# Optimization experiments

Hardware: AMD Instinct MI355X
Metric: run time of the kernel (lower is better)

The kernel has to match this reference:

```python
import jax, jax.numpy as jnp
from jax import lax
import numpy as np

B, L, C_IN, HID, RANK, NC = 256, 1024, 16, 512, 128, 10
PAD, K = 4, 7  # each conv block: L -> L + 2*PAD - K + 1 = L + 2


def _block(x, dwk, dwb, pwk, pwb, g, b):
    # x: (B, C, L); depthwise conv (groups=C) -> pointwise 1x1 -> batchnorm (batch stats) -> relu
    cin = dwk.shape[0]
    dn = ('NCH', 'OIH', 'NCH')
    y = lax.conv_general_dilated(x, dwk, (1,), [(PAD, PAD)], dimension_numbers=dn,
                                 feature_group_count=cin) + dwb[None, :, None]
    y = lax.conv_general_dilated(y, pwk, (1,), [(0, 0)], dimension_numbers=dn) + pwb[None, :, None]
    m = y.mean(axis=(0, 2), keepdims=True)
    v = y.var(axis=(0, 2), keepdims=True)
    y = (y - m) * lax.rsqrt(v + 1e-5) * g[None, :, None] + b[None, :, None]
    return jax.nn.relu(y)


def _cell(xp, h, c, Ui, Vi, Uh, Vh, bi, bh):
    # low-rank LSTM cell: W = U @ V kept factored for efficiency (same math)
    gates = (xp @ Ui) @ Vi + bi + (h @ Uh) @ Vh + bh  # (B, 4H)
    i, f, g, o = jnp.split(gates, 4, axis=1)
    c = jax.nn.sigmoid(f) * c + jax.nn.sigmoid(i) * jnp.tanh(g)
    h = jax.nn.sigmoid(o) * jnp.tanh(c)
    return h, c


def _forward(x, dw_k1, dw_b1, pw_k1, pw_b1, bn_g1, bn_b1,
             dw_k2, dw_b2, pw_k2, pw_b2, bn_g2, bn_b2,
             dw_k3, dw_b3, pw_k3, pw_b3, bn_g3, bn_b3,
             dw_k4, dw_b4, pw_k4, pw_b4, bn_g4, bn_b4,
             Ui1, Vi1, Uh1, Vh1, bi1, bh1,
             Ui2, Vi2, Uh2, Vh2, bi2, bh2,
             fc_w, fc_b):
    y = x[:, 0].transpose(0, 2, 1)  # (B, C_IN, L)
    y = _block(y, dw_k1, dw_b1, pw_k1, pw_b1, bn_g1, bn_b1)
    y = _block(y, dw_k2, dw_b2, pw_k2, pw_b2, bn_g2, bn_b2)
    y = _block(y, dw_k3, dw_b3, pw_k3, pw_b3, bn_g3, bn_b3)
    y = _block(y, dw_k4, dw_b4, pw_k4, pw_b4, bn_g4, bn_b4)
    # dropout = identity (eval)
    xs = y.transpose(2, 0, 1)  # (T, B, 32), T = L + 8
    bsz = xs.shape[1]
    z = jnp.zeros((bsz, HID), xs.dtype)

    def step(carry, xt):
        h1, c1, h2, c2 = carry
        h1, c1 = _cell(xt, h1, c1, Ui1, Vi1, Uh1, Vh1, bi1, bh1)
        h2, c2 = _cell(h1, h2, c2, Ui2, Vi2, Uh2, Vh2, bi2, bh2)
        return (h1, c1, h2, c2), None

    (h1, c1, h2, c2), _ = lax.scan(step, (z, z, z, z), xs)
    # original stacks all h2 then takes [:, -1, :] -> final h2; dropout = identity
    return h2 @ fc_w.T + fc_b  # (B, NC)


def setup_inputs() -> dict:
    key = jax.random.key(0)
    ks = iter(jax.random.split(key, 64))

    def n(shape, scale=0.05):
        return jax.random.normal(next(ks), shape, jnp.float32) * scale

    inp = {'x': jax.random.normal(next(ks), (B, 1, L, C_IN), jnp.float32)}
    chans = [C_IN, 32, 32, 32]
    for i, cin in enumerate(chans, start=1):
        inp[f'dw_k{i}'] = n((cin, 1, K))
        inp[f'dw_b{i}'] = jnp.zeros((cin,), jnp.float32)
        inp[f'pw_k{i}'] = n((32, cin, 1))
        inp[f'pw_b{i}'] = jnp.zeros((32,), jnp.float32)
        inp[f'bn_g{i}'] = jnp.ones((32,), jnp.float32)
        inp[f'bn_b{i}'] = jnp.zeros((32,), jnp.float32)
    inp['Ui1'] = n((32, RANK)); inp['Vi1'] = n((RANK, 4 * HID))
    inp['Uh1'] = n((HID, RANK)); inp['Vh1'] = n((RANK, 4 * HID))
    inp['bi1'] = jnp.zeros((4 * HID,), jnp.float32); inp['bh1'] = jnp.zeros((4 * HID,), jnp.float32)
    inp['Ui2'] = n((HID, RANK)); inp['Vi2'] = n((RANK, 4 * HID))
    inp['Uh2'] = n((HID, RANK)); inp['Vh2'] = n((RANK, 4 * HID))
    inp['bi2'] = jnp.zeros((4 * HID,), jnp.float32); inp['bh2'] = jnp.zeros((4 * HID,), jnp.float32)
    inp['fc_w'] = n((NC, HID)); inp['fc_b'] = jnp.zeros((NC,), jnp.float32)
    return inp


def reference(x, dw_k1, dw_b1, pw_k1, pw_b1, bn_g1, bn_b1,
              dw_k2, dw_b2, pw_k2, pw_b2, bn_g2, bn_b2,
              dw_k3, dw_b3, pw_k3, pw_b3, bn_g3, bn_b3,
              dw_k4, dw_b4, pw_k4, pw_b4, bn_g4, bn_b4,
              Ui1, Vi1, Uh1, Vh1, bi1, bh1,
              Ui2, Vi2, Uh2, Vh2, bi2, bh2,
              fc_w, fc_b):
    return _forward(x, dw_k1, dw_b1, pw_k1, pw_b1, bn_g1, bn_b1,
                    dw_k2, dw_b2, pw_k2, pw_b2, bn_g2, bn_b2,
                    dw_k3, dw_b3, pw_k3, pw_b3, bn_g3, bn_b3,
                    dw_k4, dw_b4, pw_k4, pw_b4, bn_g4, bn_b4,
                    Ui1, Vi1, Uh1, Vh1, bi1, bh1,
                    Ui2, Vi2, Uh2, Vh2, bi2, bh2,
                    fc_w, fc_b)
```

## Files before the change

### kernel.cpp

```cpp
#include <hip/hip_runtime.h>
#include <stdint.h>
#include <stddef.h>
#include <limits.h>

typedef _Float16 f16;
typedef _Float16 half8 __attribute__((ext_vector_type(8)));
typedef float floatx4 __attribute__((ext_vector_type(4)));
typedef unsigned long long u64;

#define MFMA(a,b,c) __builtin_amdgcn_mfma_f32_16x16x32_f16((a),(b),(c),0,0,0)

static constexpr int LMAX   = 1032;
static constexpr int TSTEPS = 1032;

static constexpr size_t ZBYTES   = (size_t)256*32*LMAX*2;
static constexpr size_t OFF_ZA   = 0;
static constexpr size_t OFF_ZB   = OFF_ZA + ZBYTES;
static constexpr size_t OFF_Y4   = OFF_ZA;
static constexpr size_t OFF_WH1F = OFF_ZB + ZBYTES;
static constexpr size_t OFF_WI2F = OFF_WH1F + (size_t)128*16*64*8*2;
static constexpr size_t OFF_WH2F = OFF_WI2F + (size_t)128*16*64*8*2;
static constexpr size_t OFF_WX1F = OFF_WH2F + (size_t)128*16*64*8*2;
static constexpr size_t OFF_B1   = OFF_WX1F + (size_t)128*64*8*2;
static constexpr size_t OFF_B2   = OFF_B1 + (size_t)2048*4;
static constexpr size_t OFF_STATS= OFF_B2 + (size_t)2048*4;
static constexpr size_t OFF_AB   = OFF_STATS + (size_t)4*64*4;
static constexpr size_t OFF_H1X  = OFF_AB + (size_t)4*64*4;
static constexpr size_t OFF_H2X  = OFF_H1X + (size_t)8*8*32*512*2;
static constexpr size_t OFF_FLAGS= OFF_H2X + (size_t)8*4*32*512*2;

__device__ __forceinline__ float sigm(float x){ return 1.f/(1.f+__expf(-x)); }
__device__ __forceinline__ float tanh_f(float x){ float e=__expf(2.f*x); return (e-1.f)/(e+1.f); }

__device__ __forceinline__ void sta64(void* p, u64 v){
  __hip_atomic_store((u64*)p, v, __ATOMIC_RELAXED, __HIP_MEMORY_SCOPE_AGENT);
}
__device__ __forceinline__ u64 lda64(const void* p){
  return __hip_atomic_load((const u64*)p, __ATOMIC_RELAXED, __HIP_MEMORY_SCOPE_AGENT);
}
__device__ __forceinline__ uint32_t ldf(const uint32_t* p){
  return __hip_atomic_load(p, __ATOMIC_RELAXED, __HIP_MEMORY_SCOPE_AGENT);
}
__device__ __forceinline__ void stf(uint32_t* p, uint32_t v){
  __hip_atomic_store(p, v, __ATOMIC_RELAXED, __HIP_MEMORY_SCOPE_AGENT);
}
__device__ __forceinline__ float4 ldg16(const void* p){
  float4 r;
  asm volatile("global_load_dwordx4 %0, %1, off sc0 sc1" : "=v"(r) : "v"(p) : "memory");
  return r;
}
__device__ __forceinline__ void vmcnt0(){
  asm volatile("s_waitcnt vmcnt(0)" ::: "memory");
}

__device__ __forceinline__ void pollWave(const uint32_t* fl, int t1, int t2){
  const int lane = threadIdx.x & 63;
  int tgt = (lane < 16) ? t1 : ((lane < 32) ? t2 : INT_MIN);
  if (tgt <= 0) tgt = INT_MIN;
  while (true){
    uint32_t v = ldf(&fl[lane & 31]);
    if (__all((int)v >= tgt)) break;
    __builtin_amdgcn_s_sleep(1);
  }
}

__device__ __forceinline__ void stageIssue(float4* r, const f16* src, int tid){
  #pragma unroll
  for (int i=0;i<8;++i){
    int qq = tid + 256*i;
    r[i] = ldg16(src + (size_t)qq*8);
  }
}
__device__ __forceinline__ void stageWrite(uint8_t* base, const float4* r, int tid){
  #pragma unroll
  for (int i=0;i<8;++i){
    int qq = tid + 256*i;
    int row = qq >> 6, ck = qq & 63;
    int cs = ck ^ (row & 15);
    *(float4*)(base + ((row<<6) + cs)*16) = r[i];
  }
}
__device__ __forceinline__ half8 fragLDS(const uint8_t* base, int row, int q, int lq){
  return *(const half8*)(base + (((row<<6)) + (((q<<2)+lq) ^ (row & 15)))*16);
}

__global__ void k_zero(float* stats, uint32_t* flags){
  int bx = blockIdx.x, tid = threadIdx.x;
  if (bx == 4){ if (tid < 256) stats[tid] = 0.f; }
  else flags[bx*256 + tid] = 0u;
}

__global__ __launch_bounds__(256) void k_prep_W(f16* __restrict__ dst, const float* __restrict__ U, const float* __restrict__ V){
  __shared__ float sU[64][65];
  __shared__ float sV[64][68];
  const int tid = threadIdx.x;
  const int n0 = blockIdx.x*64, k0 = blockIdx.y*64;
  const int tx = tid & 15, ty = tid >> 4;
  float acc[4][4];
  #pragma unroll
  for (int a=0;a<4;++a){ acc[a][0]=0.f; acc[a][1]=0.f; acc[a][2]=0.f; acc[a][3]=0.f; }
  for (int rc=0; rc<2; ++rc){
    __syncthreads();
    #pragma unroll
    for (int i=0;i<16;++i){
      int f = tid + 256*i;
      int row = f>>6, col = f&63;
      sU[row][col] = U[(size_t)(k0+row)*128 + rc*64 + col];
      sV[row][col] = V[(size_t)(rc*64+row)*2048 + n0 + col];
    }
    __syncthreads();
    for (int rr=0; rr<64; ++rr){
      float4 bv = *(const float4*)&sV[rr][tx*4];
      #pragma unroll
      for (int a=0;a<4;++a){
        float av = sU[ty*4+a][rr];
        acc[a][0] += av*bv.x; acc[a][1] += av*bv.y; acc[a][2] += av*bv.z; acc[a][3] += av*bv.w;
      }
    }
  }
  #pragma unroll
  for (int a=0;a<4;++a){
    int k = k0 + ty*4 + a;
    int q = k>>5, lq2 = (k>>3)&3, j = k&7;
    #pragma unroll
    for (int c=0;c<4;++c){
      int n = n0 + tx*4 + c;
      int nt = n>>4, lmn = n&15;
      dst[(((size_t)nt*16 + q)*64 + (lq2*16+lmn))*8 + j] = (f16)acc[a][c];
    }
  }
}

__global__ __launch_bounds__(256) void k_prep_Wx(f16* __restrict__ dst, const float* __restrict__ U, const float* __restrict__ V){
  __shared__ float sU[32][129];
  __shared__ float sV[128][68];
  const int tid = threadIdx.x, n0 = blockIdx.x*64;
  for (int f=tid; f<32*128; f+=256) sU[f>>7][f&127] = U[f];
  for (int f=tid; f<128*64; f+=256) sV[f>>6][f&63] = V[(size_t)(f>>6)*2048 + n0 + (f&63)];
  __syncthreads();
  int nn = tid & 63, kb = (tid>>6)*8;
  int n = n0 + nn;
  float acc[8];
  #pragma unroll
  for (int i=0;i<8;++i) acc[i]=0.f;
  for (int r=0;r<128;++r){
    float v = sV[r][nn];
    #pragma unroll
    for (int i=0;i<8;++i) acc[i] += sU[kb+i][r]*v;
  }
  int nt = n>>4, lmn = n&15;
  #pragma unroll
  for (int i=0;i<8;++i){
    int k = kb+i;
    dst[((size_t)nt*64 + (((k>>3)&3)*16 + lmn))*8 + (k&7)] = (f16)acc[i];
  }
}

__global__ void k_prep_bias(float* dst, const float* a, const float* b){
  int idx = blockIdx.x*256 + threadIdx.x;
  if (idx < 2048) dst[idx] = a[idx] + b[idx];
}

__global__ __launch_bounds__(256) void k_conv(
    const float* __restrict__ x0, const f16* __restrict__ zin,
    const float* __restrict__ abp,
    const float* __restrict__ dwk, const float* __restrict__ dwb,
    const float* __restrict__ pwk, const float* __restrict__ pwb,
    f16* __restrict__ zout, float* __restrict__ stats,
    int Lin, int Cin)
{
  const int tid = threadIdx.x;
  const int b = blockIdx.y;
  const int l = blockIdx.x*256 + tid;
  const int Lout = Lin + 2;
  __shared__ float sPw[32*32], sDw[32*7], sDb[32], sPb[32], sAb[64];
  __shared__ float sRed[2][4][32];
  for (int i=tid; i<Cin*32; i+=256) sPw[i] = pwk[i];
  for (int i=tid; i<Cin*7;  i+=256) sDw[i] = dwk[i];
  if (tid < Cin) sDb[tid] = dwb[tid];
  if (tid >= 64 && tid < 96) sPb[tid-64] = pwb[tid-64];
  if (abp != nullptr && tid >= 128 && tid < 192) sAb[tid-128] = abp[tid-128];
  __syncthreads();

  float acc[32];
  #pragma unroll
  for (int o=0;o<32;++o) acc[o] = sPb[o];
  const bool act = (l < Lout);
  if (act){
    for (int c=0;c<Cin;++c){
      float s = sDb[c];
      #pragma unroll
      for (int k=0;k<7;++k){
        int li = l + k - 4;
        float v = 0.f;
        if (li >= 0 && li < Lin){
          if (x0) v = x0[((size_t)b*1024 + li)*16 + c];
          else {
            float z = (float)zin[((size_t)b*32 + c)*LMAX + li];
            v = fmaxf(sAb[c]*z + sAb[32+c], 0.f);
          }
        }
        s += sDw[c*7+k]*v;
      }
      #pragma unroll
      for (int o=0;o<32;++o) acc[o] += sPw[o*Cin + c]*s;
    }
    #pragma unroll
    for (int o=0;o<32;++o) zout[((size_t)b*32 + o)*LMAX + l] = (f16)acc[o];
  }
  const int lane = tid & 63, wv = tid >> 6;
  for (int o=0;o<32;++o){
    float v = act ? acc[o] : 0.f;
    float q = v*v;
    #pragma unroll
    for (int m=1;m<64;m<<=1){ v += __shfl_xor(v,m); q += __shfl_xor(q,m); }
    if (lane == 0){ sRed[0][wv][o] = v; sRed[1][wv][o] = q; }
  }
  __syncthreads();
  if (tid < 32){
    float v = sRed[0][0][tid]+sRed[0][1][tid]+sRed[0][2][tid]+sRed[0][3][tid];
    float q = sRed[1][0][tid]+sRed[1][1][tid]+sRed[1][2][tid]+sRed[1][3][tid];
    atomicAdd(&stats[tid], v);
    atomicAdd(&stats[32+tid], q);
  }
}

__global__ void k_bnfin(const float* __restrict__ stats, const float* __restrict__ g,
                        const float* __restrict__ beta, float* __restrict__ ab, float inv_n)
{
  int o = threadIdx.x;
  if (o < 32){
    float m = stats[o]*inv_n;
    float var = stats[32+o]*inv_n - m*m;
    float a = g[o]*rsqrtf(var + 1e-5f);
    ab[o] = a; ab[32+o] = beta[o] - m*a;
  }
}

__global__ __launch_bounds__(256) void k_y4(const f16* __restrict__ z, const float* __restrict__ ab, f16* __restrict__ y){
  __shared__ f16 sT[32][264];
  __shared__ float sA[64];
  const int b = blockIdx.x, t0 = blockIdx.y*256, tid = threadIdx.x;
  if (tid < 64) sA[tid] = ab[tid];
  __syncthreads();
  #pragma unroll
  for (int i=0;i<8;++i){
    int f = tid + 256*i;
    int ch = f >> 6, tq = f & 63;
    int t = t0 + tq*4;
    if (t < 1032){
      u64 v = *(const u64*)(z + ((size_t)(b*32+ch)*1032 + t));
      union { u64 u; f16 h[4]; } cv; cv.u = v;
      float a = sA[ch], bb = sA[32+ch];
      #pragma unroll
      for (int j=0;j<4;++j) cv.h[j] = (f16)fmaxf(a*(float)cv.h[j] + bb, 0.f);
      *(u64*)&sT[ch][tq*4] = cv.u;
    }
  }
  __syncthreads();
  int t = t0 + tid;
  if (t < 1032){
    union { uint4 v; f16 h[8]; } o[4];
    #pragma unroll
    for (int k=0;k<4;++k)
      #pragma unroll
      for (int j=0;j<8;++j) o[k].h[j] = sT[k*8+j][t - t0];
    uint4* dst = (uint4*)(y + ((size_t)b*1032 + t)*32);
    #pragma unroll
    for (int k=0;k<4;++k) dst[k] = o[k].v;
  }
}

__global__ __launch_bounds__(256,1) void k_lstm(
  const f16* __restrict__ y4x,
  const f16* __restrict__ Wx1F, const f16* __restrict__ Wh1F,
  const f16* __restrict__ Wi2F, const f16* __restrict__ Wh2F,
  const float* __restrict__ bias1, const float* __restrict__ bias2,
  f16* __restrict__ h1x, f16* __restrict__ h2x,
  uint32_t* __restrict__ flags,
  const float* __restrict__ fcw, const float* __restrict__ fcb,
  float* __restrict__ outp)
{
  const int tid  = threadIdx.x;
  const int lane = tid & 63;
  const int w    = tid >> 6;
  const int lm   = lane & 15;
  const int lq   = lane >> 4;
  const int lq8  = lq*8;
  const int g    = blockIdx.x & 7;
  const int idx  = blockIdx.x >> 3;
  const int role = idx >> 4;
  const int b    = idx & 15;

  __shared__ __align__(16) uint8_t bufA[32768];
  __shared__ __align__(16) uint8_t bufB[32768];
  __shared__ float sGate[4*32*33];

  uint32_t* fl = flags + (size_t)g*32;

  const float* biasL = role ? bias2 : bias1;
  float bs[2];
  #pragma unroll
  for (int ct=0; ct<2; ++ct) bs[ct] = biasL[w*512 + b*32 + ct*16 + lm];

  const int nt0 = w*32 + b*2;
  f16* hdst_base = role ? h2x + (size_t)g*4*32*512 : h1x + (size_t)g*8*32*512;

  float creg[4] = {0.f,0.f,0.f,0.f};
  const int cr_row = tid >> 3, cr_u0 = (tid & 7)*4;

  if (role == 0){
    half8 wx[2];
    half8 wB[2][16];
    #pragma unroll
    for (int ct=0; ct<2; ++ct){
      wx[ct] = *(const half8*)&Wx1F[((size_t)(nt0+ct)*64 + lane)*8];
      #pragma unroll
      for (int q=0;q<16;++q)
        wB[ct][q] = *(const half8*)&Wh1F[(((size_t)(nt0+ct)*16 + q)*64 + lane)*8];
    }
    #pragma unroll 1
    for (int t=0; t<TSTEPS; ++t){
      half8 ya0 = *(const half8*)(y4x + ((size_t)(g*32 + lm)*1032 + t)*32 + lq8);
      half8 ya1 = *(const half8*)(y4x + ((size_t)(g*32 + 16 + lm)*1032 + t)*32 + lq8);
      if (w == 0) pollWave(fl, t, t-7);
      __syncthreads();
      float4 st[8];
      if (t >= 1) stageIssue(st, h1x + ((size_t)(g*8 + ((t-1)&7))*32*512), tid);
      floatx4 acc[2][2];
      #pragma unroll
      for (int ct=0; ct<2; ++ct){
        acc[ct][0] = (floatx4){bs[ct],bs[ct],bs[ct],bs[ct]};
        acc[ct][1] = acc[ct][0];
      }
      acc[0][0] = MFMA(ya0, wx[0], acc[0][0]);
      acc[0][1] = MFMA(ya1, wx[0], acc[0][1]);
      acc[1][0] = MFMA(ya0, wx[1], acc[1][0]);
      acc[1][1] = MFMA(ya1, wx[1], acc[1][1]);
      if (t >= 1){
        vmcnt0();
        stageWrite(bufA, st, tid);
      }
      __syncthreads();
      if (t >= 1){
        #pragma unroll
        for (int q=0;q<16;++q){
          half8 a0 = fragLDS(bufA, lm,    q, lq);
          half8 a1 = fragLDS(bufA, 16+lm, q, lq);
          acc[0][0] = MFMA(a0, wB[0][q], acc[0][0]);
          acc[0][1] = MFMA(a1, wB[0][q], acc[0][1]);
          acc[1][0] = MFMA(a0, wB[1][q], acc[1][0]);
          acc[1][1] = MFMA(a1, wB[1][q], acc[1][1]);
        }
      }
      __syncthreads();
      #pragma unroll
      for (int ct=0; ct<2; ++ct)
        #pragma unroll
        for (int rt=0; rt<2; ++rt)
          #pragma unroll
          for (int r=0;r<4;++r)
            sGate[w*1056 + (rt*16 + lq*4 + r)*33 + ct*16 + lm] = acc[ct][rt][r];
      __syncthreads();
      {
        union { u64 uu; f16 h[4]; } hv;
        #pragma unroll
        for (int j=0;j<4;++j){
          int u = cr_u0 + j;
          float iv = sGate[0*1056 + cr_row*33 + u];
          float fv = sGate[1*1056 + cr_row*33 + u];
          float gv = sGate[2*1056 + cr_row*33 + u];
          float ov = sGate[3*1056 + cr_row*33 + u];
          float c = sigm(fv)*creg[j] + sigm(iv)*tanh_f(gv);
          creg[j] = c;
          hv.h[j] = (f16)(sigm(ov)*tanh_f(c));
        }
        f16* dst = hdst_base + (size_t)(t&7)*32*512 + cr_row*512 + b*32 + cr_u0;
        sta64(dst, hv.uu);
      }
      vmcnt0();
      __syncthreads();
      if (tid == 0) stf(&fl[b], (uint32_t)(t+1));
    }
  } else {
    half8 wA[2][16];
    half8 wB[2][16];
    #pragma unroll
    for (int ct=0; ct<2; ++ct)
      #pragma unroll
      for (int q=0;q<16;++q){
        wA[ct][q] = *(const half8*)&Wi2F[(((size_t)(nt0+ct)*16 + q)*64 + lane)*8];
        wB[ct][q] = *(const half8*)&Wh2F[(((size_t)(nt0+ct)*16 + q)*64 + lane)*8];
      }
    #pragma unroll 1
    for (int t=0; t<TSTEPS; ++t){
      if (w == 0) pollWave(fl, t+1, t);
      __syncthreads();
      float4 s0[8], s1[8];
      stageIssue(s0, h1x + ((size_t)(g*8 + (t&7))*32*512), tid);
      if (t >= 1) stageIssue(s1, h2x + ((size_t)(g*4 + ((t-1)&3))*32*512), tid);
      vmcnt0();
      stageWrite(bufA, s0, tid);
      if (t >= 1) stageWrite(bufB, s1, tid);
      __syncthreads();
      floatx4 acc[2][2];
      #pragma unroll
      for (int ct=0; ct<2; ++ct){
        acc[ct][0] = (floatx4){bs[ct],bs[ct],bs[ct],bs[ct]};
        acc[ct][1] = acc[ct][0];
      }
      #pragma unroll
      for (int q=0;q<16;++q){
        half8 a0 = fragLDS(bufA, lm,    q, lq);
        half8 a1 = fragLDS(bufA, 16+lm, q, lq);
        acc[0][0] = MFMA(a0, wA[0][q], acc[0][0]);
        acc[0][1] = MFMA(a1, wA[0][q], acc[0][1]);
        acc[1][0] = MFMA(a0, wA[1][q], acc[1][0]);
        acc[1][1] = MFMA(a1, wA[1][q], acc[1][1]);
      }
      if (t >= 1){
        #pragma unroll
        for (int q=0;q<16;++q){
          half8 a0 = fragLDS(bufB, lm,    q, lq);
          half8 a1 = fragLDS(bufB, 16+lm, q, lq);
          acc[0][0] = MFMA(a0, wB[0][q], acc[0][0]);
          acc[0][1] = MFMA(a1, wB[0][q], acc[0][1]);
          acc[1][0] = MFMA(a0, wB[1][q], acc[1][0]);
          acc[1][1] = MFMA(a1, wB[1][q], acc[1][1]);
        }
      }
      __syncthreads();
      #pragma unroll
      for (int ct=0; ct<2; ++ct)
        #pragma unroll
        for (int rt=0; rt<2; ++rt)
          #pragma unroll
          for (int r=0;r<4;++r)
            sGate[w*1056 + (rt*16 + lq*4 + r)*33 + ct*16 + lm] = acc[ct][rt][r];
      __syncthreads();
      {
        union { u64 uu; f16 h[4]; } hv;
        #pragma unroll
        for (int j=0;j<4;++j){
          int u = cr_u0 + j;
          float iv = sGate[0*1056 + cr_row*33 + u];
          float fv = sGate[1*1056 + cr_row*33 + u];
          float gv = sGate[2*1056 + cr_row*33 + u];
          float ov = sGate[3*1056 + cr_row*33 + u];
          float c = sigm(fv)*creg[j] + sigm(iv)*tanh_f(gv);
          creg[j] = c;
          hv.h[j] = (f16)(sigm(ov)*tanh_f(c));
        }
        f16* dst = hdst_base + (size_t)(t&3)*32*512 + cr_row*512 + b*32 + cr_u0;
        sta64(dst, hv.uu);
      }
      vmcnt0();
      __syncthreads();
      if (tid == 0) stf(&fl[16 + b], (uint32_t)(t+1));
    }
    if (b == 0){
      if (w == 0) pollWave(fl, 0, TSTEPS);
      __syncthreads();
      const f16* hbase = h2x + ((size_t)(g*4 + ((TSTEPS-1)&3))*32*512);
      for (int e = tid; e < 320; e += 256){
        int row = e/10, nc = e%10;
        float s = fcb[nc];
        const float* wv = fcw + (size_t)nc*512;
        const u64* hp = (const u64*)(hbase + row*512);
        for (int k4=0;k4<128;++k4){
          union { u64 uu; f16 h[4]; } cv; cv.uu = lda64(hp + k4);
          #pragma unroll
          for (int i2=0;i2<4;++i2) s += (float)cv.h[i2]*wv[k4*4+i2];
        }
        outp[(size_t)(g*32+row)*10 + nc] = s;
      }
    }
  }
}

extern "C" void kernel_launch(void* const* d_in, const int* in_sizes, int n_in,
                              void* d_out, int out_size, void* d_ws, size_t ws_size,
                              hipStream_t stream)
{
  (void)in_sizes; (void)n_in; (void)out_size; (void)ws_size;
  const float* x = (const float*)d_in[0];
  auto F = [&](int i){ return (const float*)d_in[i]; };
  const float *Ui1=F(25), *Vi1=F(26), *Uh1=F(27), *Vh1=F(28), *bi1=F(29), *bh1=F(30);
  const float *Ui2=F(31), *Vi2=F(32), *Uh2=F(33), *Vh2=F(34), *bi2=F(35), *bh2=F(36);
  const float *fcw=F(37), *fcb=F(38);

  uint8_t* ws = (uint8_t*)d_ws;
  f16* zA   = (f16*)(ws + OFF_ZA);
  f16* zB   = (f16*)(ws + OFF_ZB);
  f16* y4x  = (f16*)(ws + OFF_Y4);
  f16* Wh1F = (f16*)(ws + OFF_WH1F);
  f16* Wi2F = (f16*)(ws + OFF_WI2F);
  f16* Wh2F = (f16*)(ws + OFF_WH2F);
  f16* Wx1F = (f16*)(ws + OFF_WX1F);
  float* bias1 = (float*)(ws + OFF_B1);
  float* bias2 = (float*)(ws + OFF_B2);
  float* stats = (float*)(ws + OFF_STATS);
  float* ab    = (float*)(ws + OFF_AB);
  f16* h1x  = (f16*)(ws + OFF_H1X);
  f16* h2x  = (f16*)(ws + OFF_H2X);
  uint32_t* flags = (uint32_t*)(ws + OFF_FLAGS);
  float* outp = (float*)d_out;

  k_zero<<<5, 256, 0, stream>>>(stats, flags);

  k_prep_W<<<dim3(32,8), 256, 0, stream>>>(Wh1F, Uh1, Vh1);
  k_prep_W<<<dim3(32,8), 256, 0, stream>>>(Wi2F, Ui2, Vi2);
  k_prep_W<<<dim3(32,8), 256, 0, stream>>>(Wh2F, Uh2, Vh2);
  k_prep_Wx<<<32, 256, 0, stream>>>(Wx1F, Ui1, Vi1);
  k_prep_bias<<<8, 256, 0, stream>>>(bias1, bi1, bh1);
  k_prep_bias<<<8, 256, 0, stream>>>(bias2, bi2, bh2);

  dim3 cgrid(5, 256);
  k_conv<<<cgrid, 256, 0, stream>>>(x, nullptr, nullptr, F(1), F(2), F(3), F(4),
                                    zA, stats + 0*64, 1024, 16);
  k_bnfin<<<1, 64, 0, stream>>>(stats + 0*64, F(5), F(6), ab + 0*64, 1.f/(256.f*1026.f));
  k_conv<<<cgrid, 256, 0, stream>>>(nullptr, zA, ab + 0*64, F(7), F(8), F(9), F(10),
                                    zB, stats + 1*64, 1026, 32);
  k_bnfin<<<1, 64, 0, stream>>>(stats + 1*64, F(11), F(12), ab + 1*64, 1.f/(256.f*1028.f));
  k_conv<<<cgrid, 256, 0, stream>>>(nullptr, zB, ab + 1*64, F(13), F(14), F(15), F(16),
                                    zA, stats + 2*64, 1028, 32);
  k_bnfin<<<1, 64, 0, stream>>>(stats + 2*64, F(17), F(18), ab + 2*64, 1.f/(256.f*1030.f));
  k_conv<<<cgrid, 256, 0, stream>>>(nullptr, zA, ab + 2*64, F(19), F(20), F(21), F(22),
                                    zB, stats + 3*64, 1030, 32);
  k_bnfin<<<1, 64, 0, stream>>>(stats + 3*64, F(23), F(24), ab + 3*64, 1.f/(256.f*1032.f));

  k_y4<<<dim3(256,5), 256, 0, stream>>>(zB, ab + 3*64, y4x);

  k_lstm<<<256, 256, 0, stream>>>(y4x,
                                  Wx1F, Wh1F, Wi2F, Wh2F,
                                  bias1, bias2,
                                  h1x, h2x, flags,
                                  fcw, fcb, outp);
}
```

Measured before the change: 6.149 ms.

## Replace flag-based handoff with sequence-tagged ring entries in LSTM pipeline

Each hidden-state word written to the global ring buffers now carries the timestep in its upper 32 bits, so consumers poll the data itself rather than waiting for a per-block flag. This removes the producer-side vmcnt wait, barrier and flag store in layer 1, and the consumer-side flag poll before staging. Layer 2 also prefetches the h1 ring while doing its h2 MFMAs. The cost is doubled ring traffic (each 4-byte payload sits in an 8-byte word), a larger zero-init kernel for the rings, and retry loops whenever tags are stale.

```diff
diff --git a/kernel.cpp b/kernel.cpp
--- a/kernel.cpp
+++ b/kernel.cpp
@@ -26,8 +26,8 @@
 static constexpr size_t OFF_STATS= OFF_B2 + (size_t)2048*4;
 static constexpr size_t OFF_AB   = OFF_STATS + (size_t)4*64*4;
 static constexpr size_t OFF_H1X  = OFF_AB + (size_t)4*64*4;
-static constexpr size_t OFF_H2X  = OFF_H1X + (size_t)8*8*32*512*2;
-static constexpr size_t OFF_FLAGS= OFF_H2X + (size_t)8*4*32*512*2;
+static constexpr size_t OFF_H2X  = OFF_H1X + (size_t)8*8*8192*8;
+static constexpr size_t OFF_FLAGS= OFF_H2X + (size_t)8*4*8192*8;
 
 __device__ __forceinline__ float sigm(float x){ return 1.f/(1.f+__expf(-x)); }
 __device__ __forceinline__ float tanh_f(float x){ float e=__expf(2.f*x); return (e-1.f)/(e+1.f); }
@@ -44,50 +44,54 @@
 __device__ __forceinline__ void stf(uint32_t* p, uint32_t v){
   __hip_atomic_store(p, v, __ATOMIC_RELAXED, __HIP_MEMORY_SCOPE_AGENT);
 }
-__device__ __forceinline__ float4 ldg16(const void* p){
-  float4 r;
-  asm volatile("global_load_dwordx4 %0, %1, off sc0 sc1" : "=v"(r) : "v"(p) : "memory");
-  return r;
-}
-__device__ __forceinline__ void vmcnt0(){
-  asm volatile("s_waitcnt vmcnt(0)" ::: "memory");
-}
-
-__device__ __forceinline__ void pollWave(const uint32_t* fl, int t1, int t2){
+
+__device__ __forceinline__ void pollCons(const uint32_t* fl, int tgt){
   const int lane = threadIdx.x & 63;
-  int tgt = (lane < 16) ? t1 : ((lane < 32) ? t2 : INT_MIN);
-  if (tgt <= 0) tgt = INT_MIN;
+  int t2 = (lane < 16) ? tgt : INT_MIN;
   while (true){
-    uint32_t v = ldf(&fl[lane & 31]);
-    if (__all((int)v >= tgt)) break;
-    __builtin_amdgcn_s_sleep(1);
-  }
-}
-
-__device__ __forceinline__ void stageIssue(float4* r, const f16* src, int tid){
-  #pragma unroll
-  for (int i=0;i<8;++i){
-    int qq = tid + 256*i;
-    r[i] = ldg16(src + (size_t)qq*8);
-  }
-}
-__device__ __forceinline__ void stageWrite(uint8_t* base, const float4* r, int tid){
-  #pragma unroll
-  for (int i=0;i<8;++i){
-    int qq = tid + 256*i;
-    int row = qq >> 6, ck = qq & 63;
-    int cs = ck ^ (row & 15);
-    *(float4*)(base + ((row<<6) + cs)*16) = r[i];
-  }
-}
-__device__ __forceinline__ half8 fragLDS(const uint8_t* base, int row, int q, int lq){
-  return *(const half8*)(base + (((row<<6)) + (((q<<2)+lq) ^ (row & 15)))*16);
-}
-
-__global__ void k_zero(float* stats, uint32_t* flags){
+    uint32_t v = ldf(&fl[16 + (lane & 15)]);
+    if (__all((int)v >= t2)) break;
+    __builtin_amdgcn_s_sleep(2);
+  }
+}
+
+__device__ __forceinline__ void issueChunks(u64* v, const u64* slot, int tid){
+  const int base = (tid>>3)*256 + (tid&7)*2;
+  #pragma unroll
+  for (int i=0;i<16;++i){
+    v[2*i]   = lda64(slot + base + 16*i);
+    v[2*i+1] = lda64(slot + base + 16*i + 1);
+  }
+}
+__device__ __forceinline__ bool finishChunks(uint8_t* lds, const u64* v, int tid, uint32_t expect){
+  const int r = tid>>3, c0 = (tid&7)*2;
+  bool ok = true;
+  #pragma unroll
+  for (int i=0;i<16;++i){
+    u64 a = v[2*i], b = v[2*i+1];
+    ok &= ((uint32_t)(a>>32) == expect);
+    ok &= ((uint32_t)(b>>32) == expect);
+    *(uint2*)(lds + r*1040 + (c0 + 16*i)*4) = make_uint2((uint32_t)a, (uint32_t)b);
+  }
+  return ok;
+}
+__device__ __forceinline__ void stageLoop(uint8_t* lds, const u64* slot, int tid, uint32_t expect){
+  while (true){
+    u64 v[32];
+    issueChunks(v, slot, tid);
+    bool ok = finishChunks(lds, v, tid, expect);
+    if (__syncthreads_and(ok)) break;
+    __builtin_amdgcn_s_sleep(4);
+  }
+}
+__device__ __forceinline__ half8 fragP(const uint8_t* base, int row, int q, int lq){
+  return *(const half8*)(base + row*1040 + (((q<<2)+lq)<<4));
+}
+
+__global__ void k_zero(float* stats, uint32_t* flags, uint4* rings){
   int bx = blockIdx.x, tid = threadIdx.x;
-  if (bx == 4){ if (tid < 256) stats[tid] = 0.f; }
-  else flags[bx*256 + tid] = 0u;
+  if (bx < 1536) rings[(size_t)bx*256 + tid] = (uint4){0u,0u,0u,0u};
+  else { stats[tid] = 0.f; flags[tid] = 0u; }
 }
 
 __global__ __launch_bounds__(256) void k_prep_W(f16* __restrict__ dst, const float* __restrict__ U, const float* __restrict__ V){
@@ -276,7 +280,7 @@
   const f16* __restrict__ Wx1F, const f16* __restrict__ Wh1F,
   const f16* __restrict__ Wi2F, const f16* __restrict__ Wh2F,
   const float* __restrict__ bias1, const float* __restrict__ bias2,
-  f16* __restrict__ h1x, f16* __restrict__ h2x,
+  u64* __restrict__ h1x, u64* __restrict__ h2x,
   uint32_t* __restrict__ flags,
   const float* __restrict__ fcw, const float* __restrict__ fcb,
   float* __restrict__ outp)
@@ -292,10 +296,12 @@
   const int role = idx >> 4;
   const int b    = idx & 15;
 
-  __shared__ __align__(16) uint8_t bufA[32768];
-  __shared__ __align__(16) uint8_t bufB[32768];
+  __shared__ __align__(16) uint8_t bufA[33280];
+  __shared__ __align__(16) uint8_t bufB[33280];
   __shared__ float sGate[4*32*33];
 
+  u64* ring1 = h1x + (size_t)g*8*8192;
+  u64* ring2 = h2x + (size_t)g*4*8192;
   uint32_t* fl = flags + (size_t)g*32;
 
   const float* biasL = role ? bias2 : bias1;
@@ -304,10 +310,10 @@
   for (int ct=0; ct<2; ++ct) bs[ct] = biasL[w*512 + b*32 + ct*16 + lm];
 
   const int nt0 = w*32 + b*2;
-  f16* hdst_base = role ? h2x + (size_t)g*4*32*512 : h1x + (size_t)g*8*32*512;
 
   float creg[4] = {0.f,0.f,0.f,0.f};
   const int cr_row = tid >> 3, cr_u0 = (tid & 7)*4;
+  const int chunkBase = cr_row*256 + b*16 + (tid & 7)*2;
 
   if (role == 0){
     half8 wx[2];
@@ -323,10 +329,8 @@
     for (int t=0; t<TSTEPS; ++t){
       half8 ya0 = *(const half8*)(y4x + ((size_t)(g*32 + lm)*1032 + t)*32 + lq8);
       half8 ya1 = *(const half8*)(y4x + ((size_t)(g*32 + 16 + lm)*1032 + t)*32 + lq8);
-      if (w == 0) pollWave(fl, t, t-7);
+      if (w == 0 && t >= 8) pollCons(fl, t-7);
       __syncthreads();
-      float4 st[8];
-      if (t >= 1) stageIssue(st, h1x + ((size_t)(g*8 + ((t-1)&7))*32*512), tid);
       floatx4 acc[2][2];
       #pragma unroll
       for (int ct=0; ct<2; ++ct){
@@ -338,22 +342,17 @@
       acc[1][0] = MFMA(ya0, wx[1], acc[1][0]);
       acc[1][1] = MFMA(ya1, wx[1], acc[1][1]);
       if (t >= 1){
-        vmcnt0();
-        stageWrite(bufA, st, tid);
-      }
-      __syncthreads();
-      if (t >= 1){
+        stageLoop(bufA, ring1 + (size_t)((t-1)&7)*8192, tid, (uint32_t)t);
         #pragma unroll
         for (int q=0;q<16;++q){
-          half8 a0 = fragLDS(bufA, lm,    q, lq);
-          half8 a1 = fragLDS(bufA, 16+lm, q, lq);
+          half8 a0 = fragP(bufA, lm,    q, lq);
+          half8 a1 = fragP(bufA, 16+lm, q, lq);
           acc[0][0] = MFMA(a0, wB[0][q], acc[0][0]);
           acc[0][1] = MFMA(a1, wB[0][q], acc[0][1]);
           acc[1][0] = MFMA(a0, wB[1][q], acc[1][0]);
           acc[1][1] = MFMA(a1, wB[1][q], acc[1][1]);
         }
       }
-      __syncthreads();
       #pragma unroll
       for (int ct=0; ct<2; ++ct)
         #pragma unroll
@@ -363,7 +362,7 @@
             sGate[w*1056 + (rt*16 + lq*4 + r)*33 + ct*16 + lm] = acc[ct][rt][r];
       __syncthreads();
       {
-        union { u64 uu; f16 h[4]; } hv;
+        union { u64 uu; f16 h[4]; uint32_t u32v[2]; } hv;
         #pragma unroll
         for (int j=0;j<4;++j){
           int u = cr_u0 + j;
@@ -375,12 +374,11 @@
           creg[j] = c;
           hv.h[j] = (f16)(sigm(ov)*tanh_f(c));
         }
-        f16* dst = hdst_base + (size_t)(t&7)*32*512 + cr_row*512 + b*32 + cr_u0;
-        sta64(dst, hv.uu);
-      }
-      vmcnt0();
-      __syncthreads();
-      if (tid == 0) stf(&fl[b], (uint32_t)(t+1));
+        u64 seqw = ((u64)(uint32_t)(t+1)) << 32;
+        u64* dst = ring1 + (size_t)(t&7)*8192 + chunkBase;
+        sta64(dst,     (u64)hv.u32v[0] | seqw);
+        sta64(dst + 1, (u64)hv.u32v[1] | seqw);
+      }
     }
   } else {
     half8 wA[2][16];
@@ -394,42 +392,40 @@
       }
     #pragma unroll 1
     for (int t=0; t<TSTEPS; ++t){
-      if (w == 0) pollWave(fl, t+1, t);
-      __syncthreads();
-      float4 s0[8], s1[8];
-      stageIssue(s0, h1x + ((size_t)(g*8 + (t&7))*32*512), tid);
-      if (t >= 1) stageIssue(s1, h2x + ((size_t)(g*4 + ((t-1)&3))*32*512), tid);
-      vmcnt0();
-      stageWrite(bufA, s0, tid);
-      if (t >= 1) stageWrite(bufB, s1, tid);
-      __syncthreads();
       floatx4 acc[2][2];
       #pragma unroll
       for (int ct=0; ct<2; ++ct){
         acc[ct][0] = (floatx4){bs[ct],bs[ct],bs[ct],bs[ct]};
         acc[ct][1] = acc[ct][0];
       }
-      #pragma unroll
-      for (int q=0;q<16;++q){
-        half8 a0 = fragLDS(bufA, lm,    q, lq);
-        half8 a1 = fragLDS(bufA, 16+lm, q, lq);
-        acc[0][0] = MFMA(a0, wA[0][q], acc[0][0]);
-        acc[0][1] = MFMA(a1, wA[0][q], acc[0][1]);
-        acc[1][0] = MFMA(a0, wA[1][q], acc[1][0]);
-        acc[1][1] = MFMA(a1, wA[1][q], acc[1][1]);
-      }
       if (t >= 1){
+        stageLoop(bufB, ring2 + (size_t)((t-1)&3)*8192, tid, (uint32_t)t);
+        u64 vh[32];
+        issueChunks(vh, ring1 + (size_t)(t&7)*8192, tid);
         #pragma unroll
         for (int q=0;q<16;++q){
-          half8 a0 = fragLDS(bufB, lm,    q, lq);
-          half8 a1 = fragLDS(bufB, 16+lm, q, lq);
+          half8 a0 = fragP(bufB, lm,    q, lq);
+          half8 a1 = fragP(bufB, 16+lm, q, lq);
           acc[0][0] = MFMA(a0, wB[0][q], acc[0][0]);
           acc[0][1] = MFMA(a1, wB[0][q], acc[0][1]);
           acc[1][0] = MFMA(a0, wB[1][q], acc[1][0]);
           acc[1][1] = MFMA(a1, wB[1][q], acc[1][1]);
         }
-      }
-      __syncthreads();
+        bool ok = finishChunks(bufA, vh, tid, (uint32_t)(t+1));
+        if (!__syncthreads_and(ok))
+          stageLoop(bufA, ring1 + (size_t)(t&7)*8192, tid, (uint32_t)(t+1));
+      } else {
+        stageLoop(bufA, ring1 + 0, tid, 1u);
+      }
+      #pragma unroll
+      for (int q=0;q<16;++q){
+        half8 a0 = fragP(bufA, lm,    q, lq);
+        half8 a1 = fragP(bufA, 16+lm, q, lq);
+        acc[0][0] = MFMA(a0, wA[0][q], acc[0][0]);
+        acc[0][1] = MFMA(a1, wA[0][q], acc[0][1]);
+        acc[1][0] = MFMA(a0, wA[1][q], acc[1][0]);
+        acc[1][1] = MFMA(a1, wA[1][q], acc[1][1]);
+      }
       #pragma unroll
       for (int ct=0; ct<2; ++ct)
         #pragma unroll
@@ -439,7 +435,7 @@
             sGate[w*1056 + (rt*16 + lq*4 + r)*33 + ct*16 + lm] = acc[ct][rt][r];
       __syncthreads();
       {
-        union { u64 uu; f16 h[4]; } hv;
+        union { u64 uu; f16 h[4]; uint32_t u32v[2]; } hv;
         #pragma unroll
         for (int j=0;j<4;++j){
           int u = cr_u0 + j;
@@ -451,27 +447,21 @@
           creg[j] = c;
           hv.h[j] = (f16)(sigm(ov)*tanh_f(c));
         }
-        f16* dst = hdst_base + (size_t)(t&3)*32*512 + cr_row*512 + b*32 + cr_u0;
-        sta64(dst, hv.uu);
-      }
-      vmcnt0();
-      __syncthreads();
+        u64 seqw = ((u64)(uint32_t)(t+1)) << 32;
+        u64* dst = ring2 + (size_t)(t&3)*8192 + chunkBase;
+        sta64(dst,     (u64)hv.u32v[0] | seqw);
+        sta64(dst + 1, (u64)hv.u32v[1] | seqw);
+      }
       if (tid == 0) stf(&fl[16 + b], (uint32_t)(t+1));
     }
     if (b == 0){
-      if (w == 0) pollWave(fl, 0, TSTEPS);
-      __syncthreads();
-      const f16* hbase = h2x + ((size_t)(g*4 + ((TSTEPS-1)&3))*32*512);
+      stageLoop(bufA, ring2 + (size_t)((TSTEPS-1)&3)*8192, tid, (uint32_t)TSTEPS);
       for (int e = tid; e < 320; e += 256){
         int row = e/10, nc = e%10;
         float s = fcb[nc];
         const float* wv = fcw + (size_t)nc*512;
-        const u64* hp = (const u64*)(hbase + row*512);
-        for (int k4=0;k4<128;++k4){
-          union { u64 uu; f16 h[4]; } cv; cv.uu = lda64(hp + k4);
-          #pragma unroll
-          for (int i2=0;i2<4;++i2) s += (float)cv.h[i2]*wv[k4*4+i2];
-        }
+        const f16* hp = (const f16*)(bufA + row*1040);
+        for (int u=0;u<512;++u) s += (float)hp[u]*wv[u];
         outp[(size_t)(g*32+row)*10 + nc] = s;
       }
     }
@@ -501,12 +491,12 @@
   float* bias2 = (float*)(ws + OFF_B2);
   float* stats = (float*)(ws + OFF_STATS);
   float* ab    = (float*)(ws + OFF_AB);
-  f16* h1x  = (f16*)(ws + OFF_H1X);
-  f16* h2x  = (f16*)(ws + OFF_H2X);
+  u64* h1x  = (u64*)(ws + OFF_H1X);
+  u64* h2x  = (u64*)(ws + OFF_H2X);
   uint32_t* flags = (uint32_t*)(ws + OFF_FLAGS);
   float* outp = (float*)d_out;
 
-  k_zero<<<5, 256, 0, stream>>>(stats, flags);
+  k_zero<<<1537, 256, 0, stream>>>(stats, flags, (uint4*)h1x);
 
   k_prep_W<<<dim3(32,8), 256, 0, stream>>>(Wh1F, Uh1, Vh1);
   k_prep_W<<<dim3(32,8), 256, 0, stream>>>(Wi2F, Ui2, Vi2);
```

New measurement: 9.389 ms. 1.53x slower.
